# Kernel tuning notes

Measured on AMD Instinct MI355X. Metric: run time of the kernel, lower is better.

## Reference

```python
import jax, jax.numpy as jnp
import numpy as np

N_NODES = 50000
N_EDGES = 1600000
IN_F = 128
OUT_F = 32
HEADS = 4
NEG_SLOPE = 0.2


def setup_inputs() -> dict:
    key = jax.random.key(0)
    ks = jax.random.split(key, 6)
    x = jax.random.normal(ks[0], (N_NODES, IN_F), dtype=jnp.float32)
    edge_index = jax.random.randint(ks[1], (2, N_EDGES), 0, N_NODES, dtype=jnp.int32)
    edge_weight = jax.random.uniform(ks[2], (N_EDGES,), dtype=jnp.float32)
    # xavier-ish scale for params
    W = jax.random.normal(ks[3], (HEADS, IN_F, OUT_F), dtype=jnp.float32) * (1.0 / np.sqrt(IN_F))
    a_src = jax.random.normal(ks[4], (HEADS, OUT_F, 1), dtype=jnp.float32) * (1.0 / np.sqrt(OUT_F))
    a_dst = jax.random.normal(ks[5], (HEADS, OUT_F, 1), dtype=jnp.float32) * (1.0 / np.sqrt(OUT_F))
    return {"x": x, "edge_index": edge_index, "edge_weight": edge_weight,
            "W": W, "a_src": a_src, "a_dst": a_dst}


def reference(x, edge_index, edge_weight, W, a_src, a_dst):
    N = x.shape[0]
    # per-head projection: [H, N, O]
    h = jnp.einsum('ni,hio->hno', x, W)
    # per-node attention terms: [H, N]
    attn_src = jnp.einsum('hno,ho->hn', h, a_src[..., 0])
    attn_dst = jnp.einsum('hno,ho->hn', h, a_dst[..., 0])
    src, dst = edge_index[0], edge_index[1]
    # per-edge logits: [H, E]
    e = attn_src[:, src] + attn_dst[:, dst]
    e = jnp.where(e >= 0, e, NEG_SLOPE * e)  # leaky relu
    e = e * edge_weight[None, :]
    # global-max stabilization (matches torch: edge_attn.max() over all elems)
    e_exp = jnp.exp(e - jnp.max(e))
    # segment softmax denominator per destination node: [H, N]
    denom = jax.vmap(lambda v: jax.ops.segment_sum(v, dst, num_segments=N))(e_exp)
    alpha = e_exp / (denom[:, dst] + 1e-10)  # [H, E]
    # weighted messages from source nodes: [H, E, O]
    msg = h[:, src] * alpha[..., None]
    # scatter-aggregate to destination nodes: [H, N, O]
    out = jax.vmap(lambda m: jax.ops.segment_sum(m, dst, num_segments=N))(msg)
    # concat heads -> [N, H*O]
    return jnp.transpose(out, (1, 0, 2)).reshape(N, HEADS * OUT_F)
```

## Files before the change

kernel.cpp:

```cpp
#include <hip/hip_runtime.h>
#include <hip/hip_bf16.h>
#include <hip/hip_fp16.h>

#define N_NODES 50000
#define N_EDGES 1600000
#define IN_F 128
#define OUT_F 32
#define HEADS 4
#define NEG_SLOPE 0.2f
#define HO (HEADS * OUT_F)

#define NBUCKET 1563
#define BBLK 256
#define EPB (N_EDGES / BBLK)
#define PROJ_BLOCKS ((N_NODES + 63) / 64)
#define SCAN_BLKS ((NBUCKET + 255) / 256)
#define AGG_BLOCKS 3125
#define AGG_WAVES (AGG_BLOCKS * 4)
#define WPITCH 136
#define BCAP 2048

typedef __attribute__((ext_vector_type(8))) short bf16x8;
typedef __attribute__((ext_vector_type(4))) float f32x4;

__device__ __forceinline__ unsigned short bf16_bits(float f) {
    union { __hip_bfloat16 b; unsigned short u; } cv;
    cv.b = __float2bfloat16(f);
    return cv.u;
}
__device__ __forceinline__ unsigned short f16_bits(float f) {
    union { __half h; unsigned short u; } cv;
    cv.h = __float2half(f);
    return cv.u;
}
__device__ __forceinline__ float f16u(unsigned short u) {
    union { unsigned short x; __half h; } cv;
    cv.x = u;
    return __half2float(cv.h);
}

__global__ __launch_bounds__(256) void k_bhist(
    const int* __restrict__ ei, int* __restrict__ bhist,
    const float* __restrict__ W, unsigned short* __restrict__ Wtg)
{
    const int blk = blockIdx.x;
    const int t = threadIdx.x;
    if (blk >= BBLK) {
        const int bp = blk - BBLK;
        #pragma unroll
        for (int i = 0; i < 8; ++i) {
            const int idx = bp * 2048 + t + i * 256;
            const int h = idx >> 12;
            const int k = (idx >> 5) & 127;
            const int o = idx & 31;
            Wtg[(size_t)(h * 32 + o) * WPITCH + k] = bf16_bits(W[idx]);
        }
        return;
    }
    __shared__ int lhist[NBUCKET];
    for (int i = t; i < NBUCKET; i += 256) lhist[i] = 0;
    __syncthreads();
    const int* dstp = ei + N_EDGES + blk * EPB;
    for (int i = t; i < EPB; i += 256)
        atomicAdd(&lhist[dstp[i] >> 5], 1);
    __syncthreads();
    int* dump = bhist + (size_t)blk * NBUCKET;
    for (int i = t; i < NBUCKET; i += 256) dump[i] = lhist[i];
}

__global__ __launch_bounds__(256, 2) void k_proj_scan(
    const float* __restrict__ x, const unsigned short* __restrict__ Wtg,
    const float* __restrict__ a_src, const float* __restrict__ a_dst,
    unsigned short* __restrict__ h_u16, float* __restrict__ attn_s4,
    float* __restrict__ attn_d4, int* __restrict__ bhist,
    int* __restrict__ btotal)
{
    __shared__ unsigned short xls[64 * WPITCH];
    __shared__ unsigned short wls[128 * WPITCH];
    const int t = threadIdx.x;

    if (blockIdx.x >= PROJ_BLOCKS) {
        const int j = (blockIdx.x - PROJ_BLOCKS) * 256 + t;
        if (j >= NBUCKET) return;
        int run = 0;
        for (int blk = 0; blk < BBLK; blk += 8) {
            int v[8];
            #pragma unroll
            for (int q = 0; q < 8; ++q)
                v[q] = bhist[(size_t)(blk + q) * NBUCKET + j];
            #pragma unroll
            for (int q = 0; q < 8; ++q) {
                const int nv = v[q];
                bhist[(size_t)(blk + q) * NBUCKET + j] = run;
                run += nv;
            }
        }
        btotal[j] = run;
        return;
    }

    const int base = blockIdx.x * 64;
    {
        const uint4* src = (const uint4*)Wtg;
        uint4* dst = (uint4*)wls;
        for (int i = t; i < 2176; i += 256) dst[i] = src[i];
    }
    {
        const float4* xsrc = (const float4*)x + (size_t)base * 32;
        #pragma unroll
        for (int i = 0; i < 8; ++i) {
            const int idx = t + i * 256;
            const int row = idx >> 5;
            const int c4 = idx & 31;
            float4 v = {0.f, 0.f, 0.f, 0.f};
            if (base + row < N_NODES) v = xsrc[row * 32 + c4];
            ushort4 o;
            o.x = bf16_bits(v.x); o.y = bf16_bits(v.y);
            o.z = bf16_bits(v.z); o.w = bf16_bits(v.w);
            *(ushort4*)&xls[row * WPITCH + c4 * 4] = o;
        }
    }
    __syncthreads();

    const int w = t >> 6;
    const int lane = t & 63;
    const int lr = lane & 15;
    const int lq = lane >> 4;

    const unsigned short* ap = &xls[(w * 16 + lr) * WPITCH + lq * 8];
    const unsigned short* bp = &wls[lr * WPITCH + lq * 8];

    f32x4 acc[8];
    #pragma unroll
    for (int ct = 0; ct < 8; ++ct) acc[ct] = (f32x4){0.f, 0.f, 0.f, 0.f};

    #pragma unroll
    for (int ks = 0; ks < 4; ++ks) {
        const bf16x8 a = *(const bf16x8*)(ap + ks * 32);
        #pragma unroll
        for (int ct = 0; ct < 8; ++ct) {
            const bf16x8 bv = *(const bf16x8*)(bp + ct * 16 * WPITCH + ks * 32);
            acc[ct] = __builtin_amdgcn_mfma_f32_16x16x32_bf16(a, bv, acc[ct], 0, 0, 0);
        }
    }

    const int nodeq = base + w * 16 + lq * 4;
    #pragma unroll
    for (int r = 0; r < 4; ++r) {
        const int node = nodeq + r;
        if (node >= N_NODES) continue;
        unsigned short* hrow = h_u16 + (size_t)node * 128 + lr;
        #pragma unroll
        for (int ct = 0; ct < 8; ++ct)
            hrow[ct * 16] = bf16_bits(acc[ct][r]);
    }

    float asv[8], adv[8];
    #pragma unroll
    for (int h = 0; h < 4; ++h) {
        asv[2 * h]     = a_src[32 * h + lr];
        asv[2 * h + 1] = a_src[32 * h + 16 + lr];
        adv[2 * h]     = a_dst[32 * h + lr];
        adv[2 * h + 1] = a_dst[32 * h + 16 + lr];
    }
    #pragma unroll
    for (int h = 0; h < 4; ++h) {
        #pragma unroll
        for (int r = 0; r < 4; ++r) {
            float ps = acc[2 * h][r] * asv[2 * h] + acc[2 * h + 1][r] * asv[2 * h + 1];
            float pd = acc[2 * h][r] * adv[2 * h] + acc[2 * h + 1][r] * adv[2 * h + 1];
            #pragma unroll
            for (int m = 8; m >= 1; m >>= 1) {
                ps += __shfl_xor(ps, m);
                pd += __shfl_xor(pd, m);
            }
            const int node = nodeq + r;
            if (lr == 0 && node < N_NODES) {
                attn_s4[node * HEADS + h] = ps;
                attn_d4[node * HEADS + h] = pd;
            }
        }
    }
}

__global__ __launch_bounds__(256) void k_bbase(
    const int* __restrict__ btotal, int* __restrict__ bbase,
    int* __restrict__ offsets)
{
    __shared__ int part[256];
    const int t = threadIdx.x;
    const int CH = 7;
    const int lo = t * CH;
    const int hi = min(lo + CH, NBUCKET);
    int s = 0;
    for (int i = lo; i < hi; ++i) s += btotal[i];
    part[t] = s;
    __syncthreads();
    for (int d = 1; d < 256; d <<= 1) {
        const int v = (t >= d) ? part[t - d] : 0;
        __syncthreads();
        part[t] += v;
        __syncthreads();
    }
    int base = (t == 0) ? 0 : part[t - 1];
    for (int i = lo; i < hi; ++i) {
        bbase[i] = base;
        base += btotal[i];
    }
    if (t == 0) offsets[N_NODES] = N_EDGES;
}

__global__ __launch_bounds__(256) void k_bscatter(
    const int* __restrict__ ei, const float* __restrict__ ew,
    const int* __restrict__ bhist, const int* __restrict__ bbase,
    uint2* __restrict__ brec64)
{
    __shared__ int cur[NBUCKET];
    const int blk = blockIdx.x;
    const int t = threadIdx.x;
    const int* row = bhist + (size_t)blk * NBUCKET;
    for (int i = t; i < NBUCKET; i += 256) cur[i] = bbase[i] + row[i];
    __syncthreads();
    const int* srcp = ei + blk * EPB;
    const int* dstp = ei + N_EDGES + blk * EPB;
    const float* wp = ew + blk * EPB;
    for (int i = t; i < EPB; i += 256) {
        const int src = srcp[i];
        const int dst = dstp[i];
        const float w = wp[i];
        const int pos = atomicAdd(&cur[dst >> 5], 1);
        brec64[pos] = make_uint2(((unsigned)src << 16) | (unsigned)f16_bits(w),
                                 (unsigned)(dst & 31));
    }
}

__global__ __launch_bounds__(256) void k_bfinish(
    const uint2* __restrict__ brec64, const int* __restrict__ bbase,
    const int* __restrict__ btotal,
    unsigned* __restrict__ rec, int* __restrict__ offsets)
{
    __shared__ uint2 stage[BCAP];
    __shared__ unsigned sorted[BCAP];
    __shared__ int bin[32], bcur[32];
    const int j = blockIdx.x;
    const int t = threadIdx.x;
    const int start = bbase[j];
    const int n = btotal[j];

    if (t < 32) bin[t] = 0;
    __syncthreads();
    for (int i = t; i < n; i += 256) {
        const uint2 v = brec64[start + i];
        stage[i] = v;
        atomicAdd(&bin[v.y], 1);
    }
    __syncthreads();
    if (t == 0) {
        int run = 0;
        #pragma unroll
        for (int b = 0; b < 32; ++b) { bcur[b] = run; run += bin[b]; }
    }
    __syncthreads();
    if (t < 32) {
        const int d = j * 32 + t;
        if (d < N_NODES) offsets[d] = start + bcur[t];
    }
    __syncthreads();
    for (int i = t; i < n; i += 256) {
        const uint2 v = stage[i];
        sorted[atomicAdd(&bcur[v.y], 1)] = v.x;
    }
    __syncthreads();
    for (int i = t; i < n; i += 256) rec[start + i] = sorted[i];
}

__global__ __launch_bounds__(256) void k_aggregate(
    const unsigned* __restrict__ rec, const int* __restrict__ offsets,
    const float* __restrict__ attn_s4, const float* __restrict__ attn_d4,
    const unsigned* __restrict__ h32, float* __restrict__ out)
{
    const int l = threadIdx.x & 63;
    const int le = l & 15;
    const int lh = l >> 4;
    const int wid = blockIdx.x * 4 + (threadIdx.x >> 6);
    const unsigned* hp = h32 + l;

    for (int dst = wid; dst < N_NODES; dst += AGG_WAVES) {
        const int beg = offsets[dst];
        const int end = offsets[dst + 1];
        const float ad = attn_d4[dst * HEADS + lh];
        float den0 = 0.f, den1 = 0.f;
        float a0 = 0.f, a1 = 0.f, b0 = 0.f, b1 = 0.f;
        for (int c = beg; c < end; c += 16) {
            const int cnt = min(16, end - c);
            unsigned pk = 0;
            if (le < cnt) {
                const unsigned u = rec[c + le];
                const int s = u >> 16;
                float lo = attn_s4[s * HEADS + lh] + ad;
                lo = ((lo >= 0.f) ? lo : NEG_SLOPE * lo) * f16u(u & 0xffffu);
                pk = (u & 0xffff0000u) | (unsigned)f16_bits(__expf(lo));
            }
            if (cnt == 16) {
                #pragma unroll
                for (int q = 0; q < 16; q += 2) {
                    const unsigned k0 = (unsigned)__shfl((int)pk, q, 16);
                    const unsigned k1 = (unsigned)__shfl((int)pk, q + 1, 16);
                    const float p0 = f16u(k0 & 0xffffu);
                    const float p1 = f16u(k1 & 0xffffu);
                    const unsigned h0 = hp[(size_t)(k0 >> 16) * 64];
                    const unsigned h1 = hp[(size_t)(k1 >> 16) * 64];
                    a0 = fmaf(p0, __uint_as_float(h0 << 16), a0);
                    b0 = fmaf(p0, __uint_as_float(h0 & 0xffff0000u), b0);
                    a1 = fmaf(p1, __uint_as_float(h1 << 16), a1);
                    b1 = fmaf(p1, __uint_as_float(h1 & 0xffff0000u), b1);
                    den0 += p0;
                    den1 += p1;
                }
            } else {
                for (int q = 0; q < cnt; ++q) {
                    const unsigned k0 = (unsigned)__shfl((int)pk, q, 16);
                    const float p0 = f16u(k0 & 0xffffu);
                    const unsigned h0 = hp[(size_t)(k0 >> 16) * 64];
                    a0 = fmaf(p0, __uint_as_float(h0 << 16), a0);
                    b0 = fmaf(p0, __uint_as_float(h0 & 0xffff0000u), b0);
                    den0 += p0;
                }
            }
        }
        const float inv = 1.f / ((den0 + den1) + 1e-10f);
        float2 o;
        o.x = (a0 + a1) * inv;
        o.y = (b0 + b1) * inv;
        ((float2*)out)[(size_t)dst * 64 + l] = o;
    }
}

extern "C" void kernel_launch(void* const* d_in, const int* in_sizes, int n_in,
                              void* d_out, int out_size, void* d_ws, size_t ws_size,
                              hipStream_t stream) {
    const float* x   = (const float*)d_in[0];
    const int*   ei  = (const int*)d_in[1];
    const float* ew  = (const float*)d_in[2];
    const float* W   = (const float*)d_in[3];
    const float* a_s = (const float*)d_in[4];
    const float* a_d = (const float*)d_in[5];
    float* out = (float*)d_out;

    unsigned* h32     = (unsigned*)d_ws;
    float*    attn_s4 = (float*)(h32 + (size_t)N_NODES * 64);
    float*    attn_d4 = attn_s4 + (size_t)N_NODES * HEADS;
    uint2*    brec64  = (uint2*)(attn_d4 + (size_t)N_NODES * HEADS);
    unsigned* rec     = (unsigned*)(brec64 + N_EDGES);
    int*      bhist   = (int*)(rec + N_EDGES);
    int*      btotal  = bhist + BBLK * NBUCKET;
    int*      bbase   = btotal + NBUCKET;
    int*      offsets = bbase + NBUCKET;
    unsigned short* Wtg = (unsigned short*)(offsets + N_NODES + 1);

    k_bhist<<<BBLK + 8, 256, 0, stream>>>(ei, bhist, W, Wtg);
    k_proj_scan<<<PROJ_BLOCKS + SCAN_BLKS, 256, 0, stream>>>(
        x, Wtg, a_s, a_d, (unsigned short*)h32, attn_s4, attn_d4,
        bhist, btotal);
    k_bbase<<<1, 256, 0, stream>>>(btotal, bbase, offsets);
    k_bscatter<<<BBLK, 256, 0, stream>>>(ei, ew, bhist, bbase, brec64);
    k_bfinish<<<NBUCKET, 256, 0, stream>>>(brec64, bbase, btotal, rec, offsets);
    k_aggregate<<<AGG_BLOCKS, 256, 0, stream>>>(rec, offsets, attn_s4,
                                                attn_d4, h32, out);
}
```

Baseline: 134.8 us.

## Split projection across scan and scatter kernels to overlap independent work

The node projection GEMM is split into two halves. The first half (391 blocks) runs alongside the bucket prefix scan. The second half runs inside the scatter kernel, next to the edge-scatter blocks. Scan blocks are moved to the front of the grid so the latency-bound scan and scatter phases share the GPU with compute work, filling idle CUs. The cost is that the scatter kernel now reserves the projection's large LDS tiles in every block, which can lower scatter occupancy.

Result: no change. 132.2 us (-1.9%).

```diff
diff --git a/kernel.cpp b/kernel.cpp
--- a/kernel.cpp
+++ b/kernel.cpp
@@ -14,6 +14,8 @@
 #define BBLK 256
 #define EPB (N_EDGES / BBLK)
 #define PROJ_BLOCKS ((N_NODES + 63) / 64)
+#define PROJ_A 391
+#define PROJ_B (PROJ_BLOCKS - PROJ_A)
 #define SCAN_BLKS ((NBUCKET + 255) / 256)
 #define AGG_BLOCKS 3125
 #define AGG_WAVES (AGG_BLOCKS * 4)
@@ -37,6 +39,97 @@
     union { unsigned short x; __half h; } cv;
     cv.x = u;
     return __half2float(cv.h);
+}
+
+__device__ __forceinline__ void proj_body(
+    int pb, int t, unsigned short* xls, unsigned short* wls,
+    const float* __restrict__ x, const unsigned short* __restrict__ Wtg,
+    const float* __restrict__ a_src, const float* __restrict__ a_dst,
+    unsigned short* __restrict__ h_u16, float* __restrict__ attn_s4,
+    float* __restrict__ attn_d4)
+{
+    const int base = pb * 64;
+    {
+        const uint4* src = (const uint4*)Wtg;
+        uint4* dst = (uint4*)wls;
+        for (int i = t; i < 2176; i += 256) dst[i] = src[i];
+    }
+    {
+        const float4* xsrc = (const float4*)x + (size_t)base * 32;
+        #pragma unroll
+        for (int i = 0; i < 8; ++i) {
+            const int idx = t + i * 256;
+            const int row = idx >> 5;
+            const int c4 = idx & 31;
+            float4 v = {0.f, 0.f, 0.f, 0.f};
+            if (base + row < N_NODES) v = xsrc[row * 32 + c4];
+            ushort4 o;
+            o.x = bf16_bits(v.x); o.y = bf16_bits(v.y);
+            o.z = bf16_bits(v.z); o.w = bf16_bits(v.w);
+            *(ushort4*)&xls[row * WPITCH + c4 * 4] = o;
+        }
+    }
+    __syncthreads();
+
+    const int w = t >> 6;
+    const int lane = t & 63;
+    const int lr = lane & 15;
+    const int lq = lane >> 4;
+
+    const unsigned short* ap = &xls[(w * 16 + lr) * WPITCH + lq * 8];
+    const unsigned short* bp = &wls[lr * WPITCH + lq * 8];
+
+    f32x4 acc[8];
+    #pragma unroll
+    for (int ct = 0; ct < 8; ++ct) acc[ct] = (f32x4){0.f, 0.f, 0.f, 0.f};
+
+    #pragma unroll
+    for (int ks = 0; ks < 4; ++ks) {
+        const bf16x8 a = *(const bf16x8*)(ap + ks * 32);
+        #pragma unroll
+        for (int ct = 0; ct < 8; ++ct) {
+            const bf16x8 bv = *(const bf16x8*)(bp + ct * 16 * WPITCH + ks * 32);
+            acc[ct] = __builtin_amdgcn_mfma_f32_16x16x32_bf16(a, bv, acc[ct], 0, 0, 0);
+        }
+    }
+
+    const int nodeq = base + w * 16 + lq * 4;
+    #pragma unroll
+    for (int r = 0; r < 4; ++r) {
+        const int node = nodeq + r;
+        if (node >= N_NODES) continue;
+        unsigned short* hrow = h_u16 + (size_t)node * 128 + lr;
+        #pragma unroll
+        for (int ct = 0; ct < 8; ++ct)
+            hrow[ct * 16] = bf16_bits(acc[ct][r]);
+    }
+
+    float asv[8], adv[8];
+    #pragma unroll
+    for (int h = 0; h < 4; ++h) {
+        asv[2 * h]     = a_src[32 * h + lr];
+        asv[2 * h + 1] = a_src[32 * h + 16 + lr];
+        adv[2 * h]     = a_dst[32 * h + lr];
+        adv[2 * h + 1] = a_dst[32 * h + 16 + lr];
+    }
+    #pragma unroll
+    for (int h = 0; h < 4; ++h) {
+        #pragma unroll
+        for (int r = 0; r < 4; ++r) {
+            float ps = acc[2 * h][r] * asv[2 * h] + acc[2 * h + 1][r] * asv[2 * h + 1];
+            float pd = acc[2 * h][r] * adv[2 * h] + acc[2 * h + 1][r] * adv[2 * h + 1];
+            #pragma unroll
+            for (int m = 8; m >= 1; m >>= 1) {
+                ps += __shfl_xor(ps, m);
+                pd += __shfl_xor(pd, m);
+            }
+            const int node = nodeq + r;
+            if (lr == 0 && node < N_NODES) {
+                attn_s4[node * HEADS + h] = ps;
+                attn_d4[node * HEADS + h] = pd;
+            }
+        }
+    }
 }
 
 __global__ __launch_bounds__(256) void k_bhist(
@@ -68,7 +161,7 @@
     for (int i = t; i < NBUCKET; i += 256) dump[i] = lhist[i];
 }
 
-__global__ __launch_bounds__(256, 2) void k_proj_scan(
+__global__ __launch_bounds__(256, 2) void k_projA_scan(
     const float* __restrict__ x, const unsigned short* __restrict__ Wtg,
     const float* __restrict__ a_src, const float* __restrict__ a_dst,
     unsigned short* __restrict__ h_u16, float* __restrict__ attn_s4,
@@ -79,8 +172,8 @@
     __shared__ unsigned short wls[128 * WPITCH];
     const int t = threadIdx.x;
 
-    if (blockIdx.x >= PROJ_BLOCKS) {
-        const int j = (blockIdx.x - PROJ_BLOCKS) * 256 + t;
+    if (blockIdx.x < SCAN_BLKS) {
+        const int j = blockIdx.x * 256 + t;
         if (j >= NBUCKET) return;
         int run = 0;
         for (int blk = 0; blk < BBLK; blk += 8) {
@@ -98,89 +191,8 @@
         btotal[j] = run;
         return;
     }
-
-    const int base = blockIdx.x * 64;
-    {
-        const uint4* src = (const uint4*)Wtg;
-        uint4* dst = (uint4*)wls;
-        for (int i = t; i < 2176; i += 256) dst[i] = src[i];
-    }
-    {
-        const float4* xsrc = (const float4*)x + (size_t)base * 32;
-        #pragma unroll
-        for (int i = 0; i < 8; ++i) {
-            const int idx = t + i * 256;
-            const int row = idx >> 5;
-            const int c4 = idx & 31;
-            float4 v = {0.f, 0.f, 0.f, 0.f};
-            if (base + row < N_NODES) v = xsrc[row * 32 + c4];
-            ushort4 o;
-            o.x = bf16_bits(v.x); o.y = bf16_bits(v.y);
-            o.z = bf16_bits(v.z); o.w = bf16_bits(v.w);
-            *(ushort4*)&xls[row * WPITCH + c4 * 4] = o;
-        }
-    }
-    __syncthreads();
-
-    const int w = t >> 6;
-    const int lane = t & 63;
-    const int lr = lane & 15;
-    const int lq = lane >> 4;
-
-    const unsigned short* ap = &xls[(w * 16 + lr) * WPITCH + lq * 8];
-    const unsigned short* bp = &wls[lr * WPITCH + lq * 8];
-
-    f32x4 acc[8];
-    #pragma unroll
-    for (int ct = 0; ct < 8; ++ct) acc[ct] = (f32x4){0.f, 0.f, 0.f, 0.f};
-
-    #pragma unroll
-    for (int ks = 0; ks < 4; ++ks) {
-        const bf16x8 a = *(const bf16x8*)(ap + ks * 32);
-        #pragma unroll
-        for (int ct = 0; ct < 8; ++ct) {
-            const bf16x8 bv = *(const bf16x8*)(bp + ct * 16 * WPITCH + ks * 32);
-            acc[ct] = __builtin_amdgcn_mfma_f32_16x16x32_bf16(a, bv, acc[ct], 0, 0, 0);
-        }
-    }
-
-    const int nodeq = base + w * 16 + lq * 4;
-    #pragma unroll
-    for (int r = 0; r < 4; ++r) {
-        const int node = nodeq + r;
-        if (node >= N_NODES) continue;
-        unsigned short* hrow = h_u16 + (size_t)node * 128 + lr;
-        #pragma unroll
-        for (int ct = 0; ct < 8; ++ct)
-            hrow[ct * 16] = bf16_bits(acc[ct][r]);
-    }
-
-    float asv[8], adv[8];
-    #pragma unroll
-    for (int h = 0; h < 4; ++h) {
-        asv[2 * h]     = a_src[32 * h + lr];
-        asv[2 * h + 1] = a_src[32 * h + 16 + lr];
-        adv[2 * h]     = a_dst[32 * h + lr];
-        adv[2 * h + 1] = a_dst[32 * h + 16 + lr];
-    }
-    #pragma unroll
-    for (int h = 0; h < 4; ++h) {
-        #pragma unroll
-        for (int r = 0; r < 4; ++r) {
-            float ps = acc[2 * h][r] * asv[2 * h] + acc[2 * h + 1][r] * asv[2 * h + 1];
-            float pd = acc[2 * h][r] * adv[2 * h] + acc[2 * h + 1][r] * adv[2 * h + 1];
-            #pragma unroll
-            for (int m = 8; m >= 1; m >>= 1) {
-                ps += __shfl_xor(ps, m);
-                pd += __shfl_xor(pd, m);
-            }
-            const int node = nodeq + r;
-            if (lr == 0 && node < N_NODES) {
-                attn_s4[node * HEADS + h] = ps;
-                attn_d4[node * HEADS + h] = pd;
-            }
-        }
-    }
+    proj_body(blockIdx.x - SCAN_BLKS, t, xls, wls,
+              x, Wtg, a_src, a_dst, h_u16, attn_s4, attn_d4);
 }
 
 __global__ __launch_bounds__(256) void k_bbase(
@@ -210,28 +222,40 @@
     if (t == 0) offsets[N_NODES] = N_EDGES;
 }
 
-__global__ __launch_bounds__(256) void k_bscatter(
+__global__ __launch_bounds__(256, 2) void k_projB_scatter(
+    const float* __restrict__ x, const unsigned short* __restrict__ Wtg,
+    const float* __restrict__ a_src, const float* __restrict__ a_dst,
+    unsigned short* __restrict__ h_u16, float* __restrict__ attn_s4,
+    float* __restrict__ attn_d4,
     const int* __restrict__ ei, const float* __restrict__ ew,
     const int* __restrict__ bhist, const int* __restrict__ bbase,
     uint2* __restrict__ brec64)
 {
+    __shared__ unsigned short xls[64 * WPITCH];
+    __shared__ unsigned short wls[128 * WPITCH];
     __shared__ int cur[NBUCKET];
-    const int blk = blockIdx.x;
-    const int t = threadIdx.x;
-    const int* row = bhist + (size_t)blk * NBUCKET;
-    for (int i = t; i < NBUCKET; i += 256) cur[i] = bbase[i] + row[i];
-    __syncthreads();
-    const int* srcp = ei + blk * EPB;
-    const int* dstp = ei + N_EDGES + blk * EPB;
-    const float* wp = ew + blk * EPB;
-    for (int i = t; i < EPB; i += 256) {
-        const int src = srcp[i];
-        const int dst = dstp[i];
-        const float w = wp[i];
-        const int pos = atomicAdd(&cur[dst >> 5], 1);
-        brec64[pos] = make_uint2(((unsigned)src << 16) | (unsigned)f16_bits(w),
-                                 (unsigned)(dst & 31));
-    }
+    const int t = threadIdx.x;
+
+    if (blockIdx.x < BBLK) {
+        const int blk = blockIdx.x;
+        const int* row = bhist + (size_t)blk * NBUCKET;
+        for (int i = t; i < NBUCKET; i += 256) cur[i] = bbase[i] + row[i];
+        __syncthreads();
+        const int* srcp = ei + blk * EPB;
+        const int* dstp = ei + N_EDGES + blk * EPB;
+        const float* wp = ew + blk * EPB;
+        for (int i = t; i < EPB; i += 256) {
+            const int src = srcp[i];
+            const int dst = dstp[i];
+            const float w = wp[i];
+            const int pos = atomicAdd(&cur[dst >> 5], 1);
+            brec64[pos] = make_uint2(((unsigned)src << 16) | (unsigned)f16_bits(w),
+                                     (unsigned)(dst & 31));
+        }
+        return;
+    }
+    proj_body(blockIdx.x - BBLK + PROJ_A, t, xls, wls,
+              x, Wtg, a_src, a_dst, h_u16, attn_s4, attn_d4);
 }
 
 __global__ __launch_bounds__(256) void k_bfinish(
@@ -359,11 +383,13 @@
     unsigned short* Wtg = (unsigned short*)(offsets + N_NODES + 1);
 
     k_bhist<<<BBLK + 8, 256, 0, stream>>>(ei, bhist, W, Wtg);
-    k_proj_scan<<<PROJ_BLOCKS + SCAN_BLKS, 256, 0, stream>>>(
+    k_projA_scan<<<SCAN_BLKS + PROJ_A, 256, 0, stream>>>(
         x, Wtg, a_s, a_d, (unsigned short*)h32, attn_s4, attn_d4,
         bhist, btotal);
     k_bbase<<<1, 256, 0, stream>>>(btotal, bbase, offsets);
-    k_bscatter<<<BBLK, 256, 0, stream>>>(ei, ew, bhist, bbase, brec64);
+    k_projB_scatter<<<BBLK + PROJ_B, 256, 0, stream>>>(
+        x, Wtg, a_s, a_d, (unsigned short*)h32, attn_s4, attn_d4,
+        ei, ew, bhist, bbase, brec64);
     k_bfinish<<<NBUCKET, 256, 0, stream>>>(brec64, bbase, btotal, rec, offsets);
     k_aggregate<<<AGG_BLOCKS, 256, 0, stream>>>(rec, offsets, attn_s4,
                                                 attn_d4, h32, out);
```
